# Performance work log

Hardware: AMD Instinct MI355X
Metric: run time of the kernel (lower is better)

Reference implementation:

```python
import jax, jax.numpy as jnp
import numpy as np

N_HEAD = 8
D_MODEL = 512
D_QKV = 64
LN_EPS = 1e-6


def setup_inputs() -> dict:
    key = jax.random.key(0)
    ks = jax.random.split(key, 10)
    B, S = 4, 2048
    q = jax.random.normal(ks[0], (B, S, D_MODEL), dtype=jnp.float32)
    k = jax.random.normal(ks[1], (B, S, D_MODEL), dtype=jnp.float32)
    v = jax.random.normal(ks[2], (B, S, D_MODEL), dtype=jnp.float32)
    mask = jax.random.randint(ks[3], (B, S, S), 0, 2, dtype=jnp.int32)
    scale = 1.0 / np.sqrt(D_MODEL)
    Wq = jax.random.normal(ks[4], (D_MODEL, N_HEAD * D_QKV), dtype=jnp.float32) * scale
    Wk = jax.random.normal(ks[5], (D_MODEL, N_HEAD * D_QKV), dtype=jnp.float32) * scale
    Wv = jax.random.normal(ks[6], (D_MODEL, N_HEAD * D_QKV), dtype=jnp.float32) * scale
    Wfc = jax.random.normal(ks[7], (N_HEAD * D_QKV, D_MODEL), dtype=jnp.float32) * scale
    gamma = jnp.ones((D_MODEL,), dtype=jnp.float32)
    beta = jnp.zeros((D_MODEL,), dtype=jnp.float32)
    return {"q": q, "k": k, "v": v, "mask": mask, "Wq": Wq, "Wk": Wk,
            "Wv": Wv, "Wfc": Wfc, "gamma": gamma, "beta": beta}


def _layer_norm(x, gamma, beta):
    mu = jnp.mean(x, axis=-1, keepdims=True)
    var = jnp.mean(jnp.square(x - mu), axis=-1, keepdims=True)
    return (x - mu) * jax.lax.rsqrt(var + LN_EPS) * gamma + beta


def reference(q, k, v, mask, Wq, Wk, Wv, Wfc, gamma, beta):
    B, Sq, _ = q.shape
    Sk = k.shape[1]
    residual = q
    qn = _layer_norm(q, gamma, beta)
    # projections -> [B, S, H, Dk]
    qh = (qn @ Wq).reshape(B, Sq, N_HEAD, D_QKV)
    kh = (k @ Wk).reshape(B, Sk, N_HEAD, D_QKV)
    vh = (v @ Wv).reshape(B, Sk, N_HEAD, D_QKV)
    temp = jnp.float32(D_QKV ** 0.5)
    # scores: [B, H, Sq, Sk]
    attn = jnp.einsum('bqhd,bkhd->bhqk', qh / temp, kh)
    attn = jnp.where(mask[:, None, :, :] == 0, jnp.float32(-1e9), attn)
    attn = jax.nn.softmax(attn, axis=-1)
    out = jnp.einsum('bhqk,bkhd->bqhd', attn, vh).reshape(B, Sq, N_HEAD * D_QKV)
    out = out @ Wfc
    return out + residual
```

## Files before the change

kernel.cpp:

```cpp
#include <hip/hip_runtime.h>

#define BATCH 4
#define SEQ   2048
#define NHEAD 8
#define DQKV  64
#define DMODEL 512
#define ROWS  (BATCH*SEQ)
#define BH    (BATCH*NHEAD)
#define HSTRIDE (SEQ*DQKV)

using f32x4  = __attribute__((ext_vector_type(4))) float;
using short8 = __attribute__((ext_vector_type(8))) short;
using short4v = __attribute__((ext_vector_type(4))) short;

#define MFMA16(a,b,c) __builtin_amdgcn_mfma_f32_16x16x32_bf16((a),(b),(c),0,0,0)

__device__ __forceinline__ short f2bf(float f) {
    unsigned u = __float_as_uint(f);
    u += 0x7FFFu + ((u >> 16) & 1u);
    return (short)(u >> 16);
}

__device__ __forceinline__ void gl2lds16(const short* g, short* l) {
    __builtin_amdgcn_global_load_lds(
        (__attribute__((address_space(1))) void*)g,
        (__attribute__((address_space(3))) void*)l, 16, 0, 0);
}

__device__ __forceinline__ void stage64x64(const short* g0, int gstride, short* lt, int t) {
    #pragma unroll
    for (int p = 0; p < 2; ++p) {
        int o = p * 2048 + t * 8;
        int row = o >> 6;
        int c = ((o >> 3) & 7) ^ (row & 7);
        gl2lds16(g0 + (size_t)row * gstride + c * 8, lt + o);
    }
}
__device__ __forceinline__ void stage128x64(const short* g0, int gstride, short* lt, int t) {
    stage64x64(g0, gstride, lt, t);
    stage64x64(g0 + (size_t)64 * gstride, gstride, lt + 4096, t);
}

__device__ __forceinline__ short8 trd(const short* t, int row, int c) {
    return *(const short8*)(t + row * 64 + ((c ^ (row & 7)) << 3));
}

__global__ __launch_bounds__(256) void prep_all_kernel(
        const float* __restrict__ q, const float* __restrict__ k,
        const float* __restrict__ v, const float* __restrict__ gamma,
        const float* __restrict__ beta, const int* __restrict__ mask,
        const float* __restrict__ W0in, const float* __restrict__ W1in,
        const float* __restrict__ W2in, const float* __restrict__ W3in,
        short* __restrict__ qn, short* __restrict__ kb, short* __restrict__ vb,
        unsigned long long* __restrict__ mp,
        short* __restrict__ T0, short* __restrict__ T1,
        short* __restrict__ T2, short* __restrict__ T3) {
    __shared__ short tile[64 * 68];
    int bid = blockIdx.x;
    int tid = threadIdx.x;
    if (bid < 4096) {
        int gw = bid * 4 + (tid >> 6);
        int lane = tid & 63;
        int lm = lane & 15, lg = lane >> 4;
        int w64 = gw & 31;
        int Qg  = (gw >> 5) & 127;
        int b   = gw >> 12;
        const int* src = mask + ((size_t)b * SEQ + Qg * 16 + lm) * SEQ + w64 * 64 + lg * 4;
        unsigned long long* d = mp + (size_t)gw * 16;
        #pragma unroll
        for (int kg = 0; kg < 4; ++kg) {
            int4 vv = *(const int4*)(src + kg * 16);
            unsigned long long w0 = __ballot(vv.x != 0);
            unsigned long long w1 = __ballot(vv.y != 0);
            unsigned long long w2 = __ballot(vv.z != 0);
            unsigned long long w3 = __ballot(vv.w != 0);
            if (lane == 0) {
                *(ulonglong2*)(d + kg*4)     = make_ulonglong2(w0, w1);
                *(ulonglong2*)(d + kg*4 + 2) = make_ulonglong2(w2, w3);
            }
        }
    } else if (bid < 8192) {
        int b2 = bid - 4096;
        const float* src = (b2 < 2048) ? k : v;
        short* dst = (b2 < 2048) ? kb : vb;
        size_t i = (size_t)(b2 & 2047) * 2048 + (size_t)tid * 8;
        float4 a = *(const float4*)(src + i);
        float4 c = *(const float4*)(src + i + 4);
        short8 o;
        o[0]=f2bf(a.x); o[1]=f2bf(a.y); o[2]=f2bf(a.z); o[3]=f2bf(a.w);
        o[4]=f2bf(c.x); o[5]=f2bf(c.y); o[6]=f2bf(c.z); o[7]=f2bf(c.w);
        *(short8*)(dst + i) = o;
    } else if (bid < 10240) {
        int wave = tid >> 6, lane = tid & 63;
        int row  = (bid - 8192) * 4 + wave;
        const float4* qr = (const float4*)(q + (size_t)row * DMODEL);
        float4 x0 = qr[lane * 2];
        float4 x1 = qr[lane * 2 + 1];
        float s  = x0.x + x0.y + x0.z + x0.w + x1.x + x1.y + x1.z + x1.w;
        float s2 = x0.x*x0.x + x0.y*x0.y + x0.z*x0.z + x0.w*x0.w
                 + x1.x*x1.x + x1.y*x1.y + x1.z*x1.z + x1.w*x1.w;
        #pragma unroll
        for (int m = 1; m < 64; m <<= 1) {
            s  += __shfl_xor(s,  m);
            s2 += __shfl_xor(s2, m);
        }
        float mu  = s * (1.0f / DMODEL);
        float var = s2 * (1.0f / DMODEL) - mu * mu;
        float rstd = rsqrtf(var + 1e-6f);
        const float4* g = (const float4*)gamma;
        const float4* be = (const float4*)beta;
        float4 g0 = g[lane*2], g1 = g[lane*2+1];
        float4 b0 = be[lane*2], b1 = be[lane*2+1];
        short8 o;
        o[0] = f2bf((x0.x - mu) * rstd * g0.x + b0.x);
        o[1] = f2bf((x0.y - mu) * rstd * g0.y + b0.y);
        o[2] = f2bf((x0.z - mu) * rstd * g0.z + b0.z);
        o[3] = f2bf((x0.w - mu) * rstd * g0.w + b0.w);
        o[4] = f2bf((x1.x - mu) * rstd * g1.x + b1.x);
        o[5] = f2bf((x1.y - mu) * rstd * g1.y + b1.y);
        o[6] = f2bf((x1.z - mu) * rstd * g1.z + b1.z);
        o[7] = f2bf((x1.w - mu) * rstd * g1.w + b1.w);
        ((short8*)(qn + (size_t)row * DMODEL))[lane] = o;
    } else {
        int b4 = bid - 10240;
        int w = b4 >> 6, ti = (b4 >> 3) & 7, tj = b4 & 7;
        const float* W = w==0 ? W0in : w==1 ? W1in : w==2 ? W2in : W3in;
        short* T = w==0 ? T0 : w==1 ? T1 : w==2 ? T2 : T3;
        #pragma unroll
        for (int p = 0; p < 4; ++p) {
            int idx = tid + p * 256;
            int kl = idx >> 4, c4 = idx & 15;
            float4 f = *(const float4*)(W + (size_t)(tj*64 + kl) * DMODEL + ti*64 + c4*4);
            short4v sv; sv[0]=f2bf(f.x); sv[1]=f2bf(f.y); sv[2]=f2bf(f.z); sv[3]=f2bf(f.w);
            *(short4v*)(tile + kl*68 + c4*4) = sv;
        }
        __syncthreads();
        #pragma unroll
        for (int p = 0; p < 4; ++p) {
            int idx = tid + p * 256;
            int nl = idx >> 4, kseg = idx & 15;
            short4v sv;
            #pragma unroll
            for (int i = 0; i < 4; ++i) sv[i] = tile[(kseg*4 + i)*68 + nl];
            *(short4v*)(T + (size_t)(ti*64 + nl) * DMODEL + tj*64 + kseg*4) = sv;
        }
    }
}

__global__ __launch_bounds__(256, 4) void proj_qkv_kernel(
        const short* __restrict__ qn, const short* __restrict__ kb,
        const short* __restrict__ vb,
        const short* __restrict__ Wqt, const short* __restrict__ Wkt,
        const short* __restrict__ Wvt,
        short* __restrict__ qhp, short* __restrict__ khp, short* __restrict__ vtp) {
    __shared__ __align__(16) short Wl[2 * 8192];
    int tid = threadIdx.x, wave = tid >> 6, lane = tid & 63;
    int lm = lane & 15, lg = lane >> 4;
    int which = blockIdx.y >> 2;
    int CB0 = (blockIdx.y & 3) * 128;
    const short* A  = which==0 ? qn  : which==1 ? kb  : vb;
    const short* Wt = which==0 ? Wqt : which==1 ? Wkt : Wvt;
    float scale = which==0 ? 0.18033688f : 1.0f;

    int RBw = blockIdx.x * 128 + wave * 32;
    const short* Arow0 = A + (size_t)(RBw + lm) * DMODEL;
    const short* Arow1 = A + (size_t)(RBw + 16 + lm) * DMODEL;
    const short* W0 = Wt + (size_t)CB0 * DMODEL;

    short8 a[2][2];
    a[0][0] = *(const short8*)(Arow0 + lg * 8);
    a[0][1] = *(const short8*)(Arow0 + 32 + lg * 8);
    a[1][0] = *(const short8*)(Arow1 + lg * 8);
    a[1][1] = *(const short8*)(Arow1 + 32 + lg * 8);
    stage128x64(W0, DMODEL, Wl, tid);
    __syncthreads();

    f32x4 acc[2][8] = {};
    for (int kk = 0; kk < DMODEL; kk += 64) {
        int cur = (kk >> 6) & 1;
        bool more = (kk + 64) < DMODEL;
        short8 an[2][2];
        if (more) {
            stage128x64(W0 + kk + 64, DMODEL, Wl + (cur ^ 1) * 8192, tid);
            an[0][0] = *(const short8*)(Arow0 + kk + 64 + lg * 8);
            an[0][1] = *(const short8*)(Arow0 + kk + 96 + lg * 8);
            an[1][0] = *(const short8*)(Arow1 + kk + 64 + lg * 8);
            an[1][1] = *(const short8*)(Arow1 + kk + 96 + lg * 8);
        }
        const short* Wc = Wl + cur * 8192;
        #pragma unroll
        for (int cg = 0; cg < 8; ++cg) {
            short8 b0 = trd(Wc, cg*16 + lm, lg);
            short8 b1 = trd(Wc, cg*16 + lm, lg + 4);
            #pragma unroll
            for (int rg = 0; rg < 2; ++rg) {
                acc[rg][cg] = MFMA16(a[rg][0], b0, acc[rg][cg]);
                acc[rg][cg] = MFMA16(a[rg][1], b1, acc[rg][cg]);
            }
        }
        if (more) {
            #pragma unroll
            for (int rg = 0; rg < 2; ++rg) { a[rg][0] = an[rg][0]; a[rg][1] = an[rg][1]; }
        }
        __syncthreads();
    }

    if (which < 2) {
        short* outh = which==0 ? qhp : khp;
        #pragma unroll
        for (int rg = 0; rg < 2; ++rg) {
            #pragma unroll
            for (int cg = 0; cg < 8; ++cg) {
                int n = CB0 + cg * 16 + lm;
                int h = n >> 6, d = n & 63;
                #pragma unroll
                for (int r = 0; r < 4; ++r) {
                    int m = RBw + rg * 16 + lg * 4 + r;
                    int bb = m >> 11, s = m & 2047;
                    outh[(size_t)(bb * NHEAD + h) * HSTRIDE + (size_t)s * DQKV + d] =
                        f2bf(acc[rg][cg][r] * scale);
                }
            }
        }
    } else {
        int bb = RBw >> 11;
        #pragma unroll
        for (int rg = 0; rg < 2; ++rg) {
            int s0 = (RBw + rg * 16 + lg * 4) & 2047;
            int s6 = s0 & 63;
            int pos = (s0 & ~63) | (s6 & 32) | ((s6 & 12) << 1) | ((s6 & 16) >> 2);
            #pragma unroll
            for (int cg = 0; cg < 8; ++cg) {
                int n = CB0 + cg * 16 + lm;
                int h = n >> 6, d = n & 63;
                short4v pk;
                #pragma unroll
                for (int r = 0; r < 4; ++r) pk[r] = f2bf(acc[rg][cg][r]);
                *(short4v*)(vtp + (size_t)(bb * NHEAD + h) * HSTRIDE
                            + (size_t)d * SEQ + pos) = pk;
            }
        }
    }
}

__global__ __launch_bounds__(256, 2) void attn_kernel(
        const short* __restrict__ qh, const short* __restrict__ kh,
        const short* __restrict__ vt, const unsigned long long* __restrict__ mpack,
        short* __restrict__ oh) {
    __shared__ __align__(16) short lds[16384];
    int tid = threadIdx.x, wave = tid >> 6, lane = tid & 63;
    int lm = lane & 15, lg = lane >> 4;

    int bid = blockIdx.y * gridDim.x + blockIdx.x;
    int slot = bid >> 3;
    int bh = (bid & 7) * 4 + (slot >> 4);
    int qt = slot & 15;
    int b = bh >> 3;
    int qbase = qt * 128 + wave * 32;

    const short* Kbase = kh + (size_t)bh * HSTRIDE;
    const short* Vtb   = vt + (size_t)bh * HSTRIDE;

    const short8* Qrow = (const short8*)(qh + (size_t)bh * HSTRIDE
                          + (size_t)(qbase + lm) * DQKV);
    short8 aq[2][2];
    aq[0][0] = Qrow[lg];       aq[0][1] = Qrow[lg + 4];
    aq[1][0] = Qrow[128 + lg]; aq[1][1] = Qrow[128 + lg + 4];

    int mb = __builtin_amdgcn_readfirstlane((b * 128 + qt * 8 + wave * 2) * 512);
    const unsigned long long* mbase = mpack + mb;

    const short one = (short)0x3F80;
    short8 ones8 = {one, one, one, one, one, one, one, one};

    f32x4 o[2][4] = {};
    f32x4 ox[2] = {};

    stage64x64(Kbase, DQKV, lds, tid);
    stage64x64(Vtb,   SEQ,  lds + 8192, tid);
    __syncthreads();

    for (int kt = 0; kt < SEQ; kt += 64) {
        int cur = (kt >> 6) & 1;
        if (kt + 64 < SEQ) {
            int nxt = cur ^ 1;
            stage64x64(Kbase + (size_t)(kt + 64) * DQKV, DQKV, lds + nxt * 4096, tid);
            stage64x64(Vtb + kt + 64, SEQ, lds + 8192 + nxt * 4096, tid);
        }
        const short* Kc = lds + cur * 4096;
        const short* Vc = lds + 8192 + cur * 4096;
        const unsigned long long* mw = mbase + (kt >> 6) * 16;

        f32x4 sk[2][4];
        #pragma unroll
        for (int kg = 0; kg < 4; ++kg) {
            short8 ak0 = trd(Kc, kg * 16 + lm, lg);
            short8 ak1 = trd(Kc, kg * 16 + lm, lg + 4);
            #pragma unroll
            for (int qg = 0; qg < 2; ++qg) {
                f32x4 z{};
                z = MFMA16(ak0, aq[qg][0], z);
                sk[qg][kg] = MFMA16(ak1, aq[qg][1], z);
            }
        }

        short8 pa8[2][2];
        #pragma unroll
        for (int qg = 0; qg < 2; ++qg) {
            #pragma unroll
            for (int kgp = 0; kgp < 2; ++kgp) {
                float p[8];
                #pragma unroll
                for (int jj = 0; jj < 8; ++jj) {
                    int kg = kgp * 2 + (jj >> 2), r = jj & 3;
                    unsigned long long mword = mw[qg * 512 + kg * 4 + r];
                    float e = __builtin_amdgcn_exp2f(sk[qg][kg][r]);
                    asm("v_cndmask_b32 %0, 0, %1, %2" : "=v"(p[jj]) : "v"(e), "s"(mword));
                }
                int w0, w1, w2, w3;
                asm("v_cvt_pk_bf16_f32 %0, %1, %2" : "=v"(w0) : "v"(p[0]), "v"(p[1]));
                asm("v_cvt_pk_bf16_f32 %0, %1, %2" : "=v"(w1) : "v"(p[2]), "v"(p[3]));
                asm("v_cvt_pk_bf16_f32 %0, %1, %2" : "=v"(w2) : "v"(p[4]), "v"(p[5]));
                asm("v_cvt_pk_bf16_f32 %0, %1, %2" : "=v"(w3) : "v"(p[6]), "v"(p[7]));
                union { int wi[4]; short8 s; } u;
                u.wi[0] = w0; u.wi[1] = w1; u.wi[2] = w2; u.wi[3] = w3;
                pa8[qg][kgp] = u.s;
            }
        }

        #pragma unroll
        for (int dt = 0; dt < 4; ++dt) {
            #pragma unroll
            for (int kgp = 0; kgp < 2; ++kgp) {
                short8 bv = trd(Vc, dt * 16 + lm, kgp * 4 + lg);
                o[0][dt] = MFMA16(pa8[0][kgp], bv, o[0][dt]);
                o[1][dt] = MFMA16(pa8[1][kgp], bv, o[1][dt]);
            }
        }
        #pragma unroll
        for (int qg = 0; qg < 2; ++qg) {
            ox[qg] = MFMA16(pa8[qg][0], ones8, ox[qg]);
            ox[qg] = MFMA16(pa8[qg][1], ones8, ox[qg]);
        }
        __syncthreads();
    }

    short* ob = oh + (size_t)bh * HSTRIDE;
    #pragma unroll
    for (int qg = 0; qg < 2; ++qg) {
        float rinv[4];
        #pragma unroll
        for (int r = 0; r < 4; ++r) rinv[r] = __builtin_amdgcn_rcpf(ox[qg][r]);
        #pragma unroll
        for (int dt = 0; dt < 4; ++dt) {
            #pragma unroll
            for (int r = 0; r < 4; ++r) {
                ob[(size_t)(qbase + qg * 16 + lg * 4 + r) * DQKV + dt * 16 + lm] =
                    f2bf(o[qg][dt][r] * rinv[r]);
            }
        }
    }
}

__global__ __launch_bounds__(256, 4) void outproj_kernel(
        const short* __restrict__ Ah, const short* __restrict__ Wfct,
        const float* __restrict__ resid, float* __restrict__ out) {
    __shared__ __align__(16) short Wl[2 * 4096];
    int tid = threadIdx.x, wave = tid >> 6, lane = tid & 63;
    int lm = lane & 15, lg = lane >> 4;
    int CB0 = blockIdx.y * 64;
    int RB = blockIdx.x * 128 + wave * 32;
    const short* W0 = Wfct + (size_t)CB0 * DMODEL;

    int m0 = RB + lm, m1 = RB + 16 + lm;
    size_t rb0 = (size_t)(m0 >> 11) * (NHEAD * HSTRIDE) + (size_t)(m0 & 2047) * DQKV;
    size_t rb1 = (size_t)(m1 >> 11) * (NHEAD * HSTRIDE) + (size_t)(m1 & 2047) * DQKV;

    short8 a[2][2];
    a[0][0] = *(const short8*)(Ah + rb0 + lg * 8);
    a[0][1] = *(const short8*)(Ah + rb0 + 32 + lg * 8);
    a[1][0] = *(const short8*)(Ah + rb1 + lg * 8);
    a[1][1] = *(const short8*)(Ah + rb1 + 32 + lg * 8);
    stage64x64(W0, DMODEL, Wl, tid);
    __syncthreads();

    f32x4 acc[2][4] = {};
    for (int kk = 0; kk < DMODEL; kk += 64) {
        int cur = (kk >> 6) & 1;
        bool more = (kk + 64) < DMODEL;
        short8 an[2][2];
        if (more) {
            stage64x64(W0 + kk + 64, DMODEL, Wl + (cur ^ 1) * 4096, tid);
            size_t hoff = (size_t)((kk >> 6) + 1) * HSTRIDE;
            an[0][0] = *(const short8*)(Ah + rb0 + hoff + lg * 8);
            an[0][1] = *(const short8*)(Ah + rb0 + hoff + 32 + lg * 8);
            an[1][0] = *(const short8*)(Ah + rb1 + hoff + lg * 8);
            an[1][1] = *(const short8*)(Ah + rb1 + hoff + 32 + lg * 8);
        }
        const short* Wc = Wl + cur * 4096;
        #pragma unroll
        for (int cg = 0; cg < 4; ++cg) {
            short8 b0 = trd(Wc, cg*16 + lm, lg);
            short8 b1 = trd(Wc, cg*16 + lm, lg + 4);
            #pragma unroll
            for (int rg = 0; rg < 2; ++rg) {
                acc[rg][cg] = MFMA16(a[rg][0], b0, acc[rg][cg]);
                acc[rg][cg] = MFMA16(a[rg][1], b1, acc[rg][cg]);
            }
        }
        if (more) {
            #pragma unroll
            for (int rg = 0; rg < 2; ++rg) { a[rg][0] = an[rg][0]; a[rg][1] = an[rg][1]; }
        }
        __syncthreads();
    }

    #pragma unroll
    for (int rg = 0; rg < 2; ++rg) {
        #pragma unroll
        for (int cg = 0; cg < 4; ++cg) {
            int n = CB0 + cg * 16 + lm;
            #pragma unroll
            for (int r = 0; r < 4; ++r) {
                int m = RB + rg * 16 + lg * 4 + r;
                size_t idx = (size_t)m * DMODEL + n;
                out[idx] = acc[rg][cg][r] + resid[idx];
            }
        }
    }
}

extern "C" void kernel_launch(void* const* d_in, const int* in_sizes, int n_in,
                              void* d_out, int out_size, void* d_ws, size_t ws_size,
                              hipStream_t stream) {
    const float* q     = (const float*)d_in[0];
    const float* k     = (const float*)d_in[1];
    const float* v     = (const float*)d_in[2];
    const int*   mask  = (const int*)d_in[3];
    const float* Wq    = (const float*)d_in[4];
    const float* Wk    = (const float*)d_in[5];
    const float* Wv    = (const float*)d_in[6];
    const float* Wfc   = (const float*)d_in[7];
    const float* gamma = (const float*)d_in[8];
    const float* beta  = (const float*)d_in[9];
    float* out = (float*)d_out;

    char* ws = (char*)d_ws;
    const size_t SZ_ROWS = (size_t)ROWS * DMODEL * sizeof(short);
    const size_t SZ_W    = (size_t)DMODEL * DMODEL * sizeof(short);
    short* qn   = (short*)(ws);
    short* kbf  = (short*)(ws + SZ_ROWS);
    short* vbf  = (short*)(ws + 2 * SZ_ROWS);
    short* Wqt  = (short*)(ws + 3 * SZ_ROWS);
    short* Wkt  = (short*)(ws + 3 * SZ_ROWS + SZ_W);
    short* Wvt  = (short*)(ws + 3 * SZ_ROWS + 2 * SZ_W);
    short* Wfct = (short*)(ws + 3 * SZ_ROWS + 3 * SZ_W);
    short* qhb  = (short*)(ws + 3 * SZ_ROWS + 4 * SZ_W);
    short* khb  = (short*)(ws + 4 * SZ_ROWS + 4 * SZ_W);
    short* vtb  = (short*)(ws + 5 * SZ_ROWS + 4 * SZ_W);
    unsigned long long* mpack = (unsigned long long*)(ws + 6 * SZ_ROWS + 4 * SZ_W);
    short* aout = qn;

    prep_all_kernel<<<dim3(10496), 256, 0, stream>>>(
        q, k, v, gamma, beta, mask, Wq, Wk, Wv, Wfc,
        qn, kbf, vbf, mpack, Wqt, Wkt, Wvt, Wfct);

    proj_qkv_kernel<<<dim3(ROWS / 128, 12), 256, 0, stream>>>(
        qn, kbf, vbf, Wqt, Wkt, Wvt, qhb, khb, vtb);

    attn_kernel<<<dim3(SEQ / 128, BH), 256, 0, stream>>>(qhb, khb, vtb, mpack, aout);

    outproj_kernel<<<dim3(ROWS / 128, DMODEL / 64), 256, 0, stream>>>(aout, Wfct, q, out);
}
```

Measured before the change: 244.6 us.

## Fuse K/V bf16 conversion into projection loads and move attention barrier earlier

```diff
diff --git a/kernel.cpp b/kernel.cpp
--- a/kernel.cpp
+++ b/kernel.cpp
@@ -21,6 +21,15 @@
     return (short)(u >> 16);
 }
 
+__device__ __forceinline__ short8 cvt8(const float* p) {
+    float4 a = *(const float4*)p;
+    float4 b = *(const float4*)(p + 4);
+    short8 o;
+    o[0]=f2bf(a.x); o[1]=f2bf(a.y); o[2]=f2bf(a.z); o[3]=f2bf(a.w);
+    o[4]=f2bf(b.x); o[5]=f2bf(b.y); o[6]=f2bf(b.z); o[7]=f2bf(b.w);
+    return o;
+}
+
 __device__ __forceinline__ void gl2lds16(const short* g, short* l) {
     __builtin_amdgcn_global_load_lds(
         (__attribute__((address_space(1))) void*)g,
@@ -46,13 +55,11 @@
 }
 
 __global__ __launch_bounds__(256) void prep_all_kernel(
-        const float* __restrict__ q, const float* __restrict__ k,
-        const float* __restrict__ v, const float* __restrict__ gamma,
+        const float* __restrict__ q, const float* __restrict__ gamma,
         const float* __restrict__ beta, const int* __restrict__ mask,
         const float* __restrict__ W0in, const float* __restrict__ W1in,
         const float* __restrict__ W2in, const float* __restrict__ W3in,
-        short* __restrict__ qn, short* __restrict__ kb, short* __restrict__ vb,
-        unsigned long long* __restrict__ mp,
+        short* __restrict__ qn, unsigned long long* __restrict__ mp,
         short* __restrict__ T0, short* __restrict__ T1,
         short* __restrict__ T2, short* __restrict__ T3) {
     __shared__ short tile[64 * 68];
@@ -79,20 +86,9 @@
                 *(ulonglong2*)(d + kg*4 + 2) = make_ulonglong2(w2, w3);
             }
         }
-    } else if (bid < 8192) {
-        int b2 = bid - 4096;
-        const float* src = (b2 < 2048) ? k : v;
-        short* dst = (b2 < 2048) ? kb : vb;
-        size_t i = (size_t)(b2 & 2047) * 2048 + (size_t)tid * 8;
-        float4 a = *(const float4*)(src + i);
-        float4 c = *(const float4*)(src + i + 4);
-        short8 o;
-        o[0]=f2bf(a.x); o[1]=f2bf(a.y); o[2]=f2bf(a.z); o[3]=f2bf(a.w);
-        o[4]=f2bf(c.x); o[5]=f2bf(c.y); o[6]=f2bf(c.z); o[7]=f2bf(c.w);
-        *(short8*)(dst + i) = o;
-    } else if (bid < 10240) {
+    } else if (bid < 6144) {
         int wave = tid >> 6, lane = tid & 63;
-        int row  = (bid - 8192) * 4 + wave;
+        int row  = (bid - 4096) * 4 + wave;
         const float4* qr = (const float4*)(q + (size_t)row * DMODEL);
         float4 x0 = qr[lane * 2];
         float4 x1 = qr[lane * 2 + 1];
@@ -122,7 +118,7 @@
         o[7] = f2bf((x1.w - mu) * rstd * g1.w + b1.w);
         ((short8*)(qn + (size_t)row * DMODEL))[lane] = o;
     } else {
-        int b4 = bid - 10240;
+        int b4 = bid - 6144;
         int w = b4 >> 6, ti = (b4 >> 3) & 7, tj = b4 & 7;
         const float* W = w==0 ? W0in : w==1 ? W1in : w==2 ? W2in : W3in;
         short* T = w==0 ? T0 : w==1 ? T1 : w==2 ? T2 : T3;
@@ -148,8 +144,8 @@
 }
 
 __global__ __launch_bounds__(256, 4) void proj_qkv_kernel(
-        const short* __restrict__ qn, const short* __restrict__ kb,
-        const short* __restrict__ vb,
+        const short* __restrict__ qn, const float* __restrict__ kf,
+        const float* __restrict__ vf,
         const short* __restrict__ Wqt, const short* __restrict__ Wkt,
         const short* __restrict__ Wvt,
         short* __restrict__ qhp, short* __restrict__ khp, short* __restrict__ vtp) {
@@ -158,20 +154,29 @@
     int lm = lane & 15, lg = lane >> 4;
     int which = blockIdx.y >> 2;
     int CB0 = (blockIdx.y & 3) * 128;
-    const short* A  = which==0 ? qn  : which==1 ? kb  : vb;
     const short* Wt = which==0 ? Wqt : which==1 ? Wkt : Wvt;
     float scale = which==0 ? 0.18033688f : 1.0f;
 
     int RBw = blockIdx.x * 128 + wave * 32;
-    const short* Arow0 = A + (size_t)(RBw + lm) * DMODEL;
-    const short* Arow1 = A + (size_t)(RBw + 16 + lm) * DMODEL;
+    const short* Aq0 = qn + (size_t)(RBw + lm) * DMODEL;
+    const short* Aq1 = qn + (size_t)(RBw + 16 + lm) * DMODEL;
+    const float* Af  = which==1 ? kf : vf;
+    const float* Af0 = Af + (size_t)(RBw + lm) * DMODEL;
+    const float* Af1 = Af + (size_t)(RBw + 16 + lm) * DMODEL;
     const short* W0 = Wt + (size_t)CB0 * DMODEL;
 
     short8 a[2][2];
-    a[0][0] = *(const short8*)(Arow0 + lg * 8);
-    a[0][1] = *(const short8*)(Arow0 + 32 + lg * 8);
-    a[1][0] = *(const short8*)(Arow1 + lg * 8);
-    a[1][1] = *(const short8*)(Arow1 + 32 + lg * 8);
+    if (which == 0) {
+        a[0][0] = *(const short8*)(Aq0 + lg * 8);
+        a[0][1] = *(const short8*)(Aq0 + 32 + lg * 8);
+        a[1][0] = *(const short8*)(Aq1 + lg * 8);
+        a[1][1] = *(const short8*)(Aq1 + 32 + lg * 8);
+    } else {
+        a[0][0] = cvt8(Af0 + lg * 8);
+        a[0][1] = cvt8(Af0 + 32 + lg * 8);
+        a[1][0] = cvt8(Af1 + lg * 8);
+        a[1][1] = cvt8(Af1 + 32 + lg * 8);
+    }
     stage128x64(W0, DMODEL, Wl, tid);
     __syncthreads();
 
@@ -182,10 +187,17 @@
         short8 an[2][2];
         if (more) {
             stage128x64(W0 + kk + 64, DMODEL, Wl + (cur ^ 1) * 8192, tid);
-            an[0][0] = *(const short8*)(Arow0 + kk + 64 + lg * 8);
-            an[0][1] = *(const short8*)(Arow0 + kk + 96 + lg * 8);
-            an[1][0] = *(const short8*)(Arow1 + kk + 64 + lg * 8);
-            an[1][1] = *(const short8*)(Arow1 + kk + 96 + lg * 8);
+            if (which == 0) {
+                an[0][0] = *(const short8*)(Aq0 + kk + 64 + lg * 8);
+                an[0][1] = *(const short8*)(Aq0 + kk + 96 + lg * 8);
+                an[1][0] = *(const short8*)(Aq1 + kk + 64 + lg * 8);
+                an[1][1] = *(const short8*)(Aq1 + kk + 96 + lg * 8);
+            } else {
+                an[0][0] = cvt8(Af0 + kk + 64 + lg * 8);
+                an[0][1] = cvt8(Af0 + kk + 96 + lg * 8);
+                an[1][0] = cvt8(Af1 + kk + 64 + lg * 8);
+                an[1][1] = cvt8(Af1 + kk + 96 + lg * 8);
+            }
         }
         const short* Wc = Wl + cur * 8192;
         #pragma unroll
@@ -303,6 +315,16 @@
                 sk[qg][kg] = MFMA16(ak1, aq[qg][1], z);
             }
         }
+
+        short8 bvr[8];
+        #pragma unroll
+        for (int dt = 0; dt < 4; ++dt) {
+            #pragma unroll
+            for (int kgp = 0; kgp < 2; ++kgp)
+                bvr[dt * 2 + kgp] = trd(Vc, dt * 16 + lm, kgp * 4 + lg);
+        }
+
+        __syncthreads();
 
         short8 pa8[2][2];
         #pragma unroll
@@ -332,9 +354,8 @@
         for (int dt = 0; dt < 4; ++dt) {
             #pragma unroll
             for (int kgp = 0; kgp < 2; ++kgp) {
-                short8 bv = trd(Vc, dt * 16 + lm, kgp * 4 + lg);
-                o[0][dt] = MFMA16(pa8[0][kgp], bv, o[0][dt]);
-                o[1][dt] = MFMA16(pa8[1][kgp], bv, o[1][dt]);
+                o[0][dt] = MFMA16(pa8[0][kgp], bvr[dt * 2 + kgp], o[0][dt]);
+                o[1][dt] = MFMA16(pa8[1][kgp], bvr[dt * 2 + kgp], o[1][dt]);
             }
         }
         #pragma unroll
@@ -342,7 +363,6 @@
             ox[qg] = MFMA16(pa8[qg][0], ones8, ox[qg]);
             ox[qg] = MFMA16(pa8[qg][1], ones8, ox[qg]);
         }
-        __syncthreads();
     }
 
     short* ob = oh + (size_t)bh * HSTRIDE;
@@ -449,8 +469,6 @@
     const size_t SZ_ROWS = (size_t)ROWS * DMODEL * sizeof(short);
     const size_t SZ_W    = (size_t)DMODEL * DMODEL * sizeof(short);
     short* qn   = (short*)(ws);
-    short* kbf  = (short*)(ws + SZ_ROWS);
-    short* vbf  = (short*)(ws + 2 * SZ_ROWS);
     short* Wqt  = (short*)(ws + 3 * SZ_ROWS);
     short* Wkt  = (short*)(ws + 3 * SZ_ROWS + SZ_W);
     short* Wvt  = (short*)(ws + 3 * SZ_ROWS + 2 * SZ_W);
@@ -461,12 +479,12 @@
     unsigned long long* mpack = (unsigned long long*)(ws + 6 * SZ_ROWS + 4 * SZ_W);
     short* aout = qn;
 
-    prep_all_kernel<<<dim3(10496), 256, 0, stream>>>(
-        q, k, v, gamma, beta, mask, Wq, Wk, Wv, Wfc,
-        qn, kbf, vbf, mpack, Wqt, Wkt, Wvt, Wfct);
+    prep_all_kernel<<<dim3(6400), 256, 0, stream>>>(
+        q, gamma, beta, mask, Wq, Wk, Wv, Wfc,
+        qn, mpack, Wqt, Wkt, Wvt, Wfct);
 
     proj_qkv_kernel<<<dim3(ROWS / 128, 12), 256, 0, stream>>>(
-        qn, kbf, vbf, Wqt, Wkt, Wvt, qhb, khb, vtb);
+        qn, k, v, Wqt, Wkt, Wvt, qhb, khb, vtb);
 
     attn_kernel<<<dim3(SEQ / 128, BH), 256, 0, stream>>>(qhb, khb, vtb, mpack, aout);
 
```

Measured after the change: 261.5 us. 6.9% more time.

## Move mask bit-packing from prep kernel into QKV projection kernel

Applied to the files above, without the earlier changes.

```diff
diff --git a/kernel.cpp b/kernel.cpp
--- a/kernel.cpp
+++ b/kernel.cpp
@@ -48,51 +48,28 @@
 __global__ __launch_bounds__(256) void prep_all_kernel(
         const float* __restrict__ q, const float* __restrict__ k,
         const float* __restrict__ v, const float* __restrict__ gamma,
-        const float* __restrict__ beta, const int* __restrict__ mask,
+        const float* __restrict__ beta,
         const float* __restrict__ W0in, const float* __restrict__ W1in,
         const float* __restrict__ W2in, const float* __restrict__ W3in,
         short* __restrict__ qn, short* __restrict__ kb, short* __restrict__ vb,
-        unsigned long long* __restrict__ mp,
         short* __restrict__ T0, short* __restrict__ T1,
         short* __restrict__ T2, short* __restrict__ T3) {
     __shared__ short tile[64 * 68];
     int bid = blockIdx.x;
     int tid = threadIdx.x;
     if (bid < 4096) {
-        int gw = bid * 4 + (tid >> 6);
-        int lane = tid & 63;
-        int lm = lane & 15, lg = lane >> 4;
-        int w64 = gw & 31;
-        int Qg  = (gw >> 5) & 127;
-        int b   = gw >> 12;
-        const int* src = mask + ((size_t)b * SEQ + Qg * 16 + lm) * SEQ + w64 * 64 + lg * 4;
-        unsigned long long* d = mp + (size_t)gw * 16;
-        #pragma unroll
-        for (int kg = 0; kg < 4; ++kg) {
-            int4 vv = *(const int4*)(src + kg * 16);
-            unsigned long long w0 = __ballot(vv.x != 0);
-            unsigned long long w1 = __ballot(vv.y != 0);
-            unsigned long long w2 = __ballot(vv.z != 0);
-            unsigned long long w3 = __ballot(vv.w != 0);
-            if (lane == 0) {
-                *(ulonglong2*)(d + kg*4)     = make_ulonglong2(w0, w1);
-                *(ulonglong2*)(d + kg*4 + 2) = make_ulonglong2(w2, w3);
-            }
-        }
-    } else if (bid < 8192) {
-        int b2 = bid - 4096;
-        const float* src = (b2 < 2048) ? k : v;
-        short* dst = (b2 < 2048) ? kb : vb;
-        size_t i = (size_t)(b2 & 2047) * 2048 + (size_t)tid * 8;
+        const float* src = (bid < 2048) ? k : v;
+        short* dst = (bid < 2048) ? kb : vb;
+        size_t i = (size_t)(bid & 2047) * 2048 + (size_t)tid * 8;
         float4 a = *(const float4*)(src + i);
         float4 c = *(const float4*)(src + i + 4);
         short8 o;
         o[0]=f2bf(a.x); o[1]=f2bf(a.y); o[2]=f2bf(a.z); o[3]=f2bf(a.w);
         o[4]=f2bf(c.x); o[5]=f2bf(c.y); o[6]=f2bf(c.z); o[7]=f2bf(c.w);
         *(short8*)(dst + i) = o;
-    } else if (bid < 10240) {
+    } else if (bid < 6144) {
         int wave = tid >> 6, lane = tid & 63;
-        int row  = (bid - 8192) * 4 + wave;
+        int row  = (bid - 4096) * 4 + wave;
         const float4* qr = (const float4*)(q + (size_t)row * DMODEL);
         float4 x0 = qr[lane * 2];
         float4 x1 = qr[lane * 2 + 1];
@@ -122,7 +99,7 @@
         o[7] = f2bf((x1.w - mu) * rstd * g1.w + b1.w);
         ((short8*)(qn + (size_t)row * DMODEL))[lane] = o;
     } else {
-        int b4 = bid - 10240;
+        int b4 = bid - 6144;
         int w = b4 >> 6, ti = (b4 >> 3) & 7, tj = b4 & 7;
         const float* W = w==0 ? W0in : w==1 ? W1in : w==2 ? W2in : W3in;
         short* T = w==0 ? T0 : w==1 ? T1 : w==2 ? T2 : T3;
@@ -147,22 +124,49 @@
     }
 }
 
-__global__ __launch_bounds__(256, 4) void proj_qkv_kernel(
+__global__ __launch_bounds__(256, 4) void proj_mask_kernel(
         const short* __restrict__ qn, const short* __restrict__ kb,
         const short* __restrict__ vb,
         const short* __restrict__ Wqt, const short* __restrict__ Wkt,
         const short* __restrict__ Wvt,
+        const int* __restrict__ mask, unsigned long long* __restrict__ mp,
         short* __restrict__ qhp, short* __restrict__ khp, short* __restrict__ vtp) {
     __shared__ __align__(16) short Wl[2 * 8192];
-    int tid = threadIdx.x, wave = tid >> 6, lane = tid & 63;
+    int bid = blockIdx.x;
+    int tid = threadIdx.x;
+    if (bid >= 768) {
+        int gw = (bid - 768) * 4 + (tid >> 6);
+        int lane = tid & 63;
+        int lm = lane & 15, lg = lane >> 4;
+        int w64 = gw & 31;
+        int Qg  = (gw >> 5) & 127;
+        int b   = gw >> 12;
+        const int* src = mask + ((size_t)b * SEQ + Qg * 16 + lm) * SEQ + w64 * 64 + lg * 4;
+        unsigned long long* d = mp + (size_t)gw * 16;
+        #pragma unroll
+        for (int kg = 0; kg < 4; ++kg) {
+            int4 vv = *(const int4*)(src + kg * 16);
+            unsigned long long w0 = __ballot(vv.x != 0);
+            unsigned long long w1 = __ballot(vv.y != 0);
+            unsigned long long w2 = __ballot(vv.z != 0);
+            unsigned long long w3 = __ballot(vv.w != 0);
+            if (lane == 0) {
+                *(ulonglong2*)(d + kg*4)     = make_ulonglong2(w0, w1);
+                *(ulonglong2*)(d + kg*4 + 2) = make_ulonglong2(w2, w3);
+            }
+        }
+        return;
+    }
+    int wave = tid >> 6, lane = tid & 63;
     int lm = lane & 15, lg = lane >> 4;
-    int which = blockIdx.y >> 2;
-    int CB0 = (blockIdx.y & 3) * 128;
+    int by = bid >> 6, bx = bid & 63;
+    int which = by >> 2;
+    int CB0 = (by & 3) * 128;
     const short* A  = which==0 ? qn  : which==1 ? kb  : vb;
     const short* Wt = which==0 ? Wqt : which==1 ? Wkt : Wvt;
     float scale = which==0 ? 0.18033688f : 1.0f;
 
-    int RBw = blockIdx.x * 128 + wave * 32;
+    int RBw = bx * 128 + wave * 32;
     const short* Arow0 = A + (size_t)(RBw + lm) * DMODEL;
     const short* Arow1 = A + (size_t)(RBw + 16 + lm) * DMODEL;
     const short* W0 = Wt + (size_t)CB0 * DMODEL;
@@ -461,12 +465,12 @@
     unsigned long long* mpack = (unsigned long long*)(ws + 6 * SZ_ROWS + 4 * SZ_W);
     short* aout = qn;
 
-    prep_all_kernel<<<dim3(10496), 256, 0, stream>>>(
-        q, k, v, gamma, beta, mask, Wq, Wk, Wv, Wfc,
-        qn, kbf, vbf, mpack, Wqt, Wkt, Wvt, Wfct);
-
-    proj_qkv_kernel<<<dim3(ROWS / 128, 12), 256, 0, stream>>>(
-        qn, kbf, vbf, Wqt, Wkt, Wvt, qhb, khb, vtb);
+    prep_all_kernel<<<dim3(6400), 256, 0, stream>>>(
+        q, k, v, gamma, beta, Wq, Wk, Wv, Wfc,
+        qn, kbf, vbf, Wqt, Wkt, Wvt, Wfct);
+
+    proj_mask_kernel<<<dim3(768 + 4096), 256, 0, stream>>>(
+        qn, kbf, vbf, Wqt, Wkt, Wvt, mask, mpack, qhb, khb, vtb);
 
     attn_kernel<<<dim3(SEQ / 128, BH), 256, 0, stream>>>(qhb, khb, vtb, mpack, aout);
 
```

Result: no change. 241.3 us (-1.4%).
